# Kernel optimization log

Measured on AMD Instinct MI355X. Metric: run time of the kernel, lower is better.

## Reference

```python
import jax, jax.numpy as jnp
import numpy as np

N_NODES = 50000
N_EDGES = 800000
D_FEAT = 128      # node feature dim (== coef_dim)
COEF_DIM = 128
OUT_DIM = 128     # node_layer / neighbour_layer output dim
EPS = 1e-12       # tf.math.l2_normalize epsilon


def setup_inputs() -> dict:
    key = jax.random.key(0)
    ks = jax.random.split(key, 8)
    s = 1.0 / np.sqrt(D_FEAT)
    h = jax.random.normal(ks[0], (N_NODES, D_FEAT), dtype=jnp.float32)
    src = jax.random.randint(ks[1], (N_EDGES,), 0, N_NODES, dtype=jnp.int32)
    dst = jax.random.randint(ks[2], (N_EDGES,), 0, N_NODES, dtype=jnp.int32)
    W_coef = jax.random.normal(ks[3], (D_FEAT, COEF_DIM), dtype=jnp.float32) * s
    b_coef = jnp.zeros((COEF_DIM,), dtype=jnp.float32)
    W_red = jax.random.normal(ks[4], (2 * COEF_DIM, 1), dtype=jnp.float32) * (1.0 / np.sqrt(2 * COEF_DIM))
    b_red = jnp.zeros((1,), dtype=jnp.float32)
    W_node = jax.random.normal(ks[5], (D_FEAT, OUT_DIM), dtype=jnp.float32) * s
    b_node = jnp.zeros((OUT_DIM,), dtype=jnp.float32)
    W_neigh = jax.random.normal(ks[6], (D_FEAT, OUT_DIM), dtype=jnp.float32) * s
    b_neigh = jnp.zeros((OUT_DIM,), dtype=jnp.float32)
    return {"h": h, "src": src, "dst": dst,
            "W_coef": W_coef, "b_coef": b_coef,
            "W_red": W_red, "b_red": b_red,
            "W_node": W_node, "b_node": b_node,
            "W_neigh": W_neigh, "b_neigh": b_neigh}


def reference(h, src, dst, W_coef, b_coef, W_red, b_red, W_node, b_node, W_neigh, b_neigh):
    n = h.shape[0]
    # message func: per-edge coef transform of source features (activation=None)
    q = h @ W_coef + b_coef                      # [N, C] dst-side coef features
    m = q[src]                                   # [E, C] (coef_layer(h[src]))
    # reduce func: attention score per edge from concat(dst coef, message)
    e = jnp.concatenate([q[dst], m], axis=-1) @ W_red + b_red   # [E, 1]
    e = e[:, 0]
    # softmax over incoming edges of each destination node (stable)
    emax = jax.ops.segment_max(e, dst, num_segments=n)          # [N]
    ex = jnp.exp(e - emax[dst])                                 # [E]
    denom = jax.ops.segment_sum(ex, dst, num_segments=n)        # [N]
    alpha = ex / (denom[dst] + EPS)                             # [E]
    # weighted neighbour aggregation of raw source features ('neigh' mailbox)
    agg = jax.ops.segment_sum(alpha[:, None] * h[src], dst, num_segments=n)  # [N, D]
    # new_h = concat(node_layer(h), neighbour_layer(agg))
    new_h = jnp.concatenate([h @ W_node + b_node, agg @ W_neigh + b_neigh], axis=-1)  # [N, 2*OUT]
    # tf.math.l2_normalize along last axis
    sq = jnp.sum(new_h * new_h, axis=-1, keepdims=True)
    return new_h * jax.lax.rsqrt(jnp.maximum(sq, EPS))
```

## Files before the change

kernel.cpp:

```cpp
#include <hip/hip_runtime.h>
#include <hip/hip_bf16.h>
#include <math.h>

#define N_NODES 50000
#define N_EDGES 800000
#define D_FEAT  128
#define EPSF    1e-12f

#define OFF_U2      0
#define OFF_PARTIAL 1024
#define OFF_S       4096
#define OFF_ROWPTR  204800
#define OFF_WTN     405504
#define OFF_WTG     438272
#define OFF_SSRC    471040
#define OFF_HB      3671040
#define OFF_AGGB    16471040

typedef __attribute__((ext_vector_type(8))) short bf8;
typedef __attribute__((ext_vector_type(4))) float f4;

__global__ void make_u2_kernel(const float* __restrict__ W_coef,
                               const float* __restrict__ W_red,
                               float* __restrict__ u2) {
    __shared__ float wr[128];
    int k = threadIdx.x;
    wr[k] = W_red[128 + k];
    __syncthreads();
    const float4* row = (const float4*)(W_coef + k * 128);
    float acc = 0.f;
    #pragma unroll
    for (int j = 0; j < 32; ++j) {
        float4 v = row[j];
        acc += v.x * wr[4*j] + v.y * wr[4*j+1] + v.z * wr[4*j+2] + v.w * wr[4*j+3];
    }
    u2[k] = acc;
}

__global__ __launch_bounds__(256) void prep_kernel(
        const float* __restrict__ h, const float* __restrict__ u2,
        const float* __restrict__ Wn, const float* __restrict__ Wg,
        const int* __restrict__ dst,
        float* __restrict__ s, unsigned short* __restrict__ hb,
        unsigned short* __restrict__ WtN, unsigned short* __restrict__ WtG,
        int* __restrict__ row_ptr, int* __restrict__ rank) {
    int b = blockIdx.x;
    if (b < 12500) {
        int node = b * 4 + (threadIdx.x >> 6);
        int lane = threadIdx.x & 63;
        float2 hv = ((const float2*)(h + (size_t)node * 128))[lane];
        float2 uv = ((const float2*)u2)[lane];
        float v = hv.x * uv.x + hv.y * uv.y;
        #pragma unroll
        for (int off = 32; off; off >>= 1) v += __shfl_xor(v, off);
        if (lane == 0) s[node] = v;
        __hip_bfloat162 p = __float22bfloat162_rn(hv);
        ((unsigned int*)(hb + (size_t)node * 128))[lane] = *(unsigned int*)&p;
    } else if (b < 12564) {
        int idx = (b - 12500) * 256 + threadIdx.x;
        int n = idx >> 7, k = idx & 127;
        __hip_bfloat16 a = __float2bfloat16(Wn[k * 128 + n]);
        __hip_bfloat16 g = __float2bfloat16(Wg[k * 128 + n]);
        WtN[n * 128 + k] = *(unsigned short*)&a;
        WtG[n * 128 + k] = *(unsigned short*)&g;
    } else {
        int e = (b - 12564) * 256 + threadIdx.x;
        if (e < N_EDGES) rank[e] = atomicAdd(&row_ptr[dst[e]], 1);
    }
}

__global__ __launch_bounds__(256) void reduce_kernel(const int* __restrict__ hist,
                                                     int* __restrict__ partial) {
    int gid = blockIdx.x * 256 + threadIdx.x;
    int v = (gid < N_NODES) ? hist[gid] : 0;
    #pragma unroll
    for (int off = 32; off; off >>= 1) v += __shfl_down(v, off);
    __shared__ int ws[4];
    int lane = threadIdx.x & 63, wid = threadIdx.x >> 6;
    if (lane == 0) ws[wid] = v;
    __syncthreads();
    if (threadIdx.x == 0) partial[blockIdx.x] = ws[0] + ws[1] + ws[2] + ws[3];
}

__global__ __launch_bounds__(256) void scan_partials_kernel(int* __restrict__ partial,
                                                            int nb) {
    int tid = threadIdx.x;
    int lane = tid & 63, wid = tid >> 6;
    int v = (tid < nb) ? partial[tid] : 0;
    int incl = v;
    #pragma unroll
    for (int off = 1; off < 64; off <<= 1) {
        int t = __shfl_up(incl, off);
        if (lane >= off) incl += t;
    }
    __shared__ int ws[4];
    if (lane == 63) ws[wid] = incl;
    __syncthreads();
    __shared__ int wbase[4];
    if (tid < 4) {
        int b = 0;
        for (int i = 0; i < tid; ++i) b += ws[i];
        wbase[tid] = b;
    }
    __syncthreads();
    partial[tid] = wbase[wid] + incl - v;
}

__global__ __launch_bounds__(256) void scan_apply_kernel(
        const int* __restrict__ partial,
        int* __restrict__ row_ptr) {
    int gid = blockIdx.x * 256 + threadIdx.x;
    int tid = threadIdx.x;
    int lane = tid & 63, wid = tid >> 6;
    int v = (gid < N_NODES) ? row_ptr[gid] : 0;
    int incl = v;
    #pragma unroll
    for (int off = 1; off < 64; off <<= 1) {
        int t = __shfl_up(incl, off);
        if (lane >= off) incl += t;
    }
    __shared__ int ws[4];
    if (lane == 63) ws[wid] = incl;
    __syncthreads();
    __shared__ int wbase[4];
    if (tid < 4) {
        int b = 0;
        for (int i = 0; i < tid; ++i) b += ws[i];
        wbase[tid] = b;
    }
    __syncthreads();
    int excl = partial[blockIdx.x] + wbase[wid] + incl - v;
    if (gid < N_NODES) row_ptr[gid] = excl;
    if (gid == 0) row_ptr[N_NODES] = N_EDGES;
}

__global__ __launch_bounds__(256) void scatter_kernel(
        const int* __restrict__ src, const int* __restrict__ dst,
        const int* __restrict__ rank, const int* __restrict__ row_ptr,
        int* __restrict__ ssrc) {
    int i = blockIdx.x * 256 + threadIdx.x;
    if (i < N_EDGES / 4) {
        int4 d = ((const int4*)dst)[i];
        int4 r = ((const int4*)rank)[i];
        int4 sv = ((const int4*)src)[i];
        ssrc[row_ptr[d.x] + r.x] = sv.x;
        ssrc[row_ptr[d.y] + r.y] = sv.y;
        ssrc[row_ptr[d.z] + r.z] = sv.z;
        ssrc[row_ptr[d.w] + r.w] = sv.w;
    }
}

__global__ __launch_bounds__(256) void aggregate_kernel(
        const int* __restrict__ row_ptr, const int* __restrict__ ssrc,
        const float* __restrict__ s,
        const unsigned short* __restrict__ hb,
        unsigned short* __restrict__ aggb) {
    int node = blockIdx.x * 4 + (threadIdx.x >> 6);
    int lane = threadIdx.x & 63;
    if (node >= N_NODES) return;
    int beg = row_ptr[node];
    int deg = row_ptr[node + 1] - beg;
    int q = lane >> 4, l16 = lane & 15;

    float acc[8] = {0.f, 0.f, 0.f, 0.f, 0.f, 0.f, 0.f, 0.f};
    float denom = 0.f;
    for (int base = 0; base < deg; base += 64) {
        int cnt = min(64, deg - base);
        int esrc = 0;
        float w_l = 0.f;
        if (lane < cnt) {
            esrc = ssrc[beg + base + lane];
            w_l = __expf(s[esrc]);
        }
        denom += w_l;
        int groups = (cnt + 3) >> 2;
        for (int j = 0; j < groups; ++j) {
            int e = 4 * j + q;
            int ec = min(e, cnt - 1);
            int bsrc = __shfl(esrc, ec);
            float w = __shfl(w_l, ec);
            if (e >= cnt) w = 0.f;
            uint4 hv = *(const uint4*)(hb + (size_t)bsrc * 128 + l16 * 8);
            acc[0] = fmaf(w, __uint_as_float(hv.x << 16),        acc[0]);
            acc[1] = fmaf(w, __uint_as_float(hv.x & 0xFFFF0000u), acc[1]);
            acc[2] = fmaf(w, __uint_as_float(hv.y << 16),        acc[2]);
            acc[3] = fmaf(w, __uint_as_float(hv.y & 0xFFFF0000u), acc[3]);
            acc[4] = fmaf(w, __uint_as_float(hv.z << 16),        acc[4]);
            acc[5] = fmaf(w, __uint_as_float(hv.z & 0xFFFF0000u), acc[5]);
            acc[6] = fmaf(w, __uint_as_float(hv.w << 16),        acc[6]);
            acc[7] = fmaf(w, __uint_as_float(hv.w & 0xFFFF0000u), acc[7]);
        }
    }
    #pragma unroll
    for (int i = 0; i < 8; ++i) {
        acc[i] += __shfl_xor(acc[i], 16);
        acc[i] += __shfl_xor(acc[i], 32);
    }
    #pragma unroll
    for (int off = 32; off; off >>= 1) denom += __shfl_xor(denom, off);
    float inv = 1.f / (denom + EPSF);
    if (q == 0) {
        unsigned o[4];
        #pragma unroll
        for (int i = 0; i < 4; ++i) {
            __hip_bfloat162 p = __float22bfloat162_rn(
                make_float2(acc[2*i] * inv, acc[2*i+1] * inv));
            o[i] = *(unsigned*)&p;
        }
        *(uint4*)(aggb + (size_t)node * 128 + l16 * 8) = make_uint4(o[0], o[1], o[2], o[3]);
    }
}

__global__ __launch_bounds__(256) void gemm_norm_mfma(
        const unsigned short* __restrict__ hb, const unsigned short* __restrict__ aggb,
        const unsigned short* __restrict__ WtN, const unsigned short* __restrict__ WtG,
        const float* __restrict__ b_node, const float* __restrict__ b_neigh,
        float* __restrict__ out) {
    int wave = threadIdx.x >> 6;
    int lane = threadIdx.x & 63;
    int node0 = blockIdx.x * 64 + wave * 16;
    if (node0 >= N_NODES) return;
    int quad = lane >> 4, l16 = lane & 15;
    int arow = node0 + l16;

    f4 accN[8], accG[8];
    #pragma unroll
    for (int t = 0; t < 8; ++t) {
        accN[t] = (f4){0.f, 0.f, 0.f, 0.f};
        accG[t] = (f4){0.f, 0.f, 0.f, 0.f};
    }

    #pragma unroll
    for (int kc = 0; kc < 4; ++kc) {
        int kbase = kc * 32 + quad * 8;
        bf8 aH = *(const bf8*)(hb   + (size_t)arow * 128 + kbase);
        bf8 aG = *(const bf8*)(aggb + (size_t)arow * 128 + kbase);
        #pragma unroll
        for (int t = 0; t < 8; ++t) {
            bf8 bN = *(const bf8*)(WtN + (size_t)(t * 16 + l16) * 128 + kbase);
            bf8 bG = *(const bf8*)(WtG + (size_t)(t * 16 + l16) * 128 + kbase);
            accN[t] = __builtin_amdgcn_mfma_f32_16x16x32_bf16(aH, bN, accN[t], 0, 0, 0);
            accG[t] = __builtin_amdgcn_mfma_f32_16x16x32_bf16(aG, bG, accG[t], 0, 0, 0);
        }
    }

    float ssr[4] = {0.f, 0.f, 0.f, 0.f};
    #pragma unroll
    for (int t = 0; t < 8; ++t) {
        float bn = b_node[t * 16 + l16];
        float bg = b_neigh[t * 16 + l16];
        #pragma unroll
        for (int r = 0; r < 4; ++r) {
            accN[t][r] += bn;
            accG[t][r] += bg;
            ssr[r] = fmaf(accN[t][r], accN[t][r], ssr[r]);
            ssr[r] = fmaf(accG[t][r], accG[t][r], ssr[r]);
        }
    }
    #pragma unroll
    for (int r = 0; r < 4; ++r) {
        ssr[r] += __shfl_xor(ssr[r], 1);
        ssr[r] += __shfl_xor(ssr[r], 2);
        ssr[r] += __shfl_xor(ssr[r], 4);
        ssr[r] += __shfl_xor(ssr[r], 8);
    }
    #pragma unroll
    for (int r = 0; r < 4; ++r) {
        float sc = rsqrtf(fmaxf(ssr[r], EPSF));
        size_t node = node0 + quad * 4 + r;
        float* o = out + node * 256;
        #pragma unroll
        for (int t = 0; t < 8; ++t) {
            o[t * 16 + l16]       = accN[t][r] * sc;
            o[128 + t * 16 + l16] = accG[t][r] * sc;
        }
    }
}

extern "C" void kernel_launch(void* const* d_in, const int* in_sizes, int n_in,
                              void* d_out, int out_size, void* d_ws, size_t ws_size,
                              hipStream_t stream) {
    const float* h       = (const float*)d_in[0];
    const int*   src     = (const int*)d_in[1];
    const int*   dst     = (const int*)d_in[2];
    const float* W_coef  = (const float*)d_in[3];
    const float* W_red   = (const float*)d_in[5];
    const float* W_node  = (const float*)d_in[7];
    const float* b_node  = (const float*)d_in[8];
    const float* W_neigh = (const float*)d_in[9];
    const float* b_neigh = (const float*)d_in[10];
    float* out = (float*)d_out;

    char* w = (char*)d_ws;
    float*          u2      = (float*)(w + OFF_U2);
    int*            partial = (int*)(w + OFF_PARTIAL);
    float*          s       = (float*)(w + OFF_S);
    int*            row_ptr = (int*)(w + OFF_ROWPTR);
    unsigned short* WtN     = (unsigned short*)(w + OFF_WTN);
    unsigned short* WtG     = (unsigned short*)(w + OFF_WTG);
    int*            ssrc    = (int*)(w + OFF_SSRC);
    unsigned short* hb      = (unsigned short*)(w + OFF_HB);
    unsigned short* aggb    = (unsigned short*)(w + OFF_AGGB);
    int*            rank    = (int*)(w + OFF_AGGB);

    const int NB = (N_NODES + 255) / 256;

    hipMemsetAsync(w + OFF_ROWPTR, 0, (N_NODES + 1) * sizeof(int), stream);
    make_u2_kernel<<<1, 128, 0, stream>>>(W_coef, W_red, u2);
    prep_kernel<<<15689, 256, 0, stream>>>(h, u2, W_node, W_neigh, dst,
                                           s, hb, WtN, WtG, row_ptr, rank);
    reduce_kernel<<<NB, 256, 0, stream>>>(row_ptr, partial);
    scan_partials_kernel<<<1, 256, 0, stream>>>(partial, NB);
    scan_apply_kernel<<<NB, 256, 0, stream>>>(partial, row_ptr);
    scatter_kernel<<<(N_EDGES / 4 + 255) / 256, 256, 0, stream>>>(src, dst, rank, row_ptr, ssrc);
    aggregate_kernel<<<N_NODES / 4, 256, 0, stream>>>(row_ptr, ssrc, s, hb, aggb);
    gemm_norm_mfma<<<(N_NODES + 63) / 64, 256, 0, stream>>>(
        hb, aggb, WtN, WtG, b_node, b_neigh, out);
}
```

Measured before the change: 236.4 us.

## Replace global-atomic CSR build with two-level bucketed counting sort

Builds the destination-sorted CSR with a two-pass radix-style sort instead of one global atomic per edge into row_ptr. Edges are first binned into groups of 120 destination nodes using per-chunk LDS histograms, a column scan and a coarse scatter. Each group is then sorted locally in LDS to produce row_ptr and ssrc. This removes heavily contended global atomics and the memset, at the cost of an extra bucket pass and a serial column-scan kernel. It also packs src into 16 bits, which relies on node ids staying below 65536.

```diff
diff --git a/kernel.cpp b/kernel.cpp
--- a/kernel.cpp
+++ b/kernel.cpp
@@ -7,15 +7,23 @@
 #define D_FEAT  128
 #define EPSF    1e-12f
 
+#define NPG     120
+#define NG      417
+#define CHUNK_E 4096
+#define NCHUNK  196
+
 #define OFF_U2      0
-#define OFF_PARTIAL 1024
-#define OFF_S       4096
-#define OFF_ROWPTR  204800
-#define OFF_WTN     405504
-#define OFF_WTG     438272
-#define OFF_SSRC    471040
-#define OFF_HB      3671040
-#define OFF_AGGB    16471040
+#define OFF_GPTR    1024
+#define OFF_TOT     4096
+#define OFF_S       8192
+#define OFF_ROWPTR  208896
+#define OFF_M       409600
+#define OFF_MX      737280
+#define OFF_WTN     1064960
+#define OFF_WTG     1097728
+#define OFF_SSRC    1130496
+#define OFF_HB      4330496
+#define OFF_AGGB    17130496
 
 typedef __attribute__((ext_vector_type(8))) short bf8;
 typedef __attribute__((ext_vector_type(4))) float f4;
@@ -43,7 +51,7 @@
         const int* __restrict__ dst,
         float* __restrict__ s, unsigned short* __restrict__ hb,
         unsigned short* __restrict__ WtN, unsigned short* __restrict__ WtG,
-        int* __restrict__ row_ptr, int* __restrict__ rank) {
+        int* __restrict__ M) {
     int b = blockIdx.x;
     if (b < 12500) {
         int node = b * 4 + (threadIdx.x >> 6);
@@ -64,89 +72,124 @@
         WtN[n * 128 + k] = *(unsigned short*)&a;
         WtG[n * 128 + k] = *(unsigned short*)&g;
     } else {
-        int e = (b - 12564) * 256 + threadIdx.x;
-        if (e < N_EDGES) rank[e] = atomicAdd(&row_ptr[dst[e]], 1);
-    }
-}
-
-__global__ __launch_bounds__(256) void reduce_kernel(const int* __restrict__ hist,
-                                                     int* __restrict__ partial) {
-    int gid = blockIdx.x * 256 + threadIdx.x;
-    int v = (gid < N_NODES) ? hist[gid] : 0;
-    #pragma unroll
-    for (int off = 32; off; off >>= 1) v += __shfl_down(v, off);
-    __shared__ int ws[4];
-    int lane = threadIdx.x & 63, wid = threadIdx.x >> 6;
-    if (lane == 0) ws[wid] = v;
-    __syncthreads();
-    if (threadIdx.x == 0) partial[blockIdx.x] = ws[0] + ws[1] + ws[2] + ws[3];
-}
-
-__global__ __launch_bounds__(256) void scan_partials_kernel(int* __restrict__ partial,
-                                                            int nb) {
+        __shared__ int lh[NG];
+        int chunk = b - 12564;
+        int tid = threadIdx.x;
+        for (int i = tid; i < NG; i += 256) lh[i] = 0;
+        __syncthreads();
+        int base_e = chunk * CHUNK_E;
+        #pragma unroll
+        for (int it = 0; it < CHUNK_E / 256; ++it) {
+            int e = base_e + it * 256 + tid;
+            if (e < N_EDGES) atomicAdd(&lh[(unsigned)dst[e] / NPG], 1);
+        }
+        __syncthreads();
+        for (int i = tid; i < NG; i += 256) M[chunk * NG + i] = lh[i];
+    }
+}
+
+__global__ __launch_bounds__(256) void mcol_kernel(
+        const int* __restrict__ M, int* __restrict__ Mx,
+        int* __restrict__ totals) {
+    int g = blockIdx.x * 256 + threadIdx.x;
+    if (g >= NG) return;
+    int running = 0;
+    for (int b = 0; b < NCHUNK; ++b) {
+        int v = M[b * NG + g];
+        Mx[b * NG + g] = running;
+        running += v;
+    }
+    totals[g] = running;
+}
+
+__global__ __launch_bounds__(512) void scan_gptr_kernel(
+        const int* __restrict__ totals, int* __restrict__ gptr) {
     int tid = threadIdx.x;
     int lane = tid & 63, wid = tid >> 6;
-    int v = (tid < nb) ? partial[tid] : 0;
+    int v = (tid < NG) ? totals[tid] : 0;
     int incl = v;
     #pragma unroll
     for (int off = 1; off < 64; off <<= 1) {
         int t = __shfl_up(incl, off);
         if (lane >= off) incl += t;
     }
-    __shared__ int ws[4];
+    __shared__ int ws[8];
     if (lane == 63) ws[wid] = incl;
     __syncthreads();
-    __shared__ int wbase[4];
-    if (tid < 4) {
+    __shared__ int wbase[8];
+    if (tid < 8) {
         int b = 0;
         for (int i = 0; i < tid; ++i) b += ws[i];
         wbase[tid] = b;
     }
     __syncthreads();
-    partial[tid] = wbase[wid] + incl - v;
-}
-
-__global__ __launch_bounds__(256) void scan_apply_kernel(
-        const int* __restrict__ partial,
-        int* __restrict__ row_ptr) {
-    int gid = blockIdx.x * 256 + threadIdx.x;
-    int tid = threadIdx.x;
+    if (tid <= NG) {
+        if (tid < NG) gptr[tid] = wbase[wid] + incl - v;
+    }
+    if (tid == 0) gptr[NG] = N_EDGES;
+}
+
+__global__ __launch_bounds__(256) void coarse_scatter_kernel(
+        const int* __restrict__ src, const int* __restrict__ dst,
+        const int* __restrict__ Mx, const int* __restrict__ gptr,
+        int* __restrict__ bucket) {
+    __shared__ int base[NG];
+    __shared__ int cnt[NG];
+    int b = blockIdx.x, tid = threadIdx.x;
+    for (int i = tid; i < NG; i += 256) {
+        base[i] = Mx[b * NG + i] + gptr[i];
+        cnt[i] = 0;
+    }
+    __syncthreads();
+    int base_e = b * CHUNK_E;
+    #pragma unroll
+    for (int it = 0; it < CHUNK_E / 256; ++it) {
+        int e = base_e + it * 256 + tid;
+        if (e < N_EDGES) {
+            int d = dst[e];
+            int g = (unsigned)d / NPG;
+            int r = atomicAdd(&cnt[g], 1);
+            bucket[base[g] + r] = src[e] | ((d - g * NPG) << 16);
+        }
+    }
+}
+
+__global__ __launch_bounds__(128) void fine_kernel(
+        const int* __restrict__ gptr, const int* __restrict__ bucket,
+        int* __restrict__ row_ptr, int* __restrict__ ssrc) {
+    __shared__ int cnt[NPG];
+    __shared__ int cnt2[NPG];
+    __shared__ int sexcl[NPG];
+    __shared__ int ws[2];
+    int g = blockIdx.x, tid = threadIdx.x;
+    if (tid < NPG) { cnt[tid] = 0; cnt2[tid] = 0; }
+    __syncthreads();
+    int beg = gptr[g], end = gptr[g + 1];
+    for (int i = beg + tid; i < end; i += 128)
+        atomicAdd(&cnt[bucket[i] >> 16], 1);
+    __syncthreads();
     int lane = tid & 63, wid = tid >> 6;
-    int v = (gid < N_NODES) ? row_ptr[gid] : 0;
+    int v = (tid < NPG) ? cnt[tid] : 0;
     int incl = v;
     #pragma unroll
     for (int off = 1; off < 64; off <<= 1) {
         int t = __shfl_up(incl, off);
         if (lane >= off) incl += t;
     }
-    __shared__ int ws[4];
     if (lane == 63) ws[wid] = incl;
     __syncthreads();
-    __shared__ int wbase[4];
-    if (tid < 4) {
-        int b = 0;
-        for (int i = 0; i < tid; ++i) b += ws[i];
-        wbase[tid] = b;
-    }
-    __syncthreads();
-    int excl = partial[blockIdx.x] + wbase[wid] + incl - v;
-    if (gid < N_NODES) row_ptr[gid] = excl;
-    if (gid == 0) row_ptr[N_NODES] = N_EDGES;
-}
-
-__global__ __launch_bounds__(256) void scatter_kernel(
-        const int* __restrict__ src, const int* __restrict__ dst,
-        const int* __restrict__ rank, const int* __restrict__ row_ptr,
-        int* __restrict__ ssrc) {
-    int i = blockIdx.x * 256 + threadIdx.x;
-    if (i < N_EDGES / 4) {
-        int4 d = ((const int4*)dst)[i];
-        int4 r = ((const int4*)rank)[i];
-        int4 sv = ((const int4*)src)[i];
-        ssrc[row_ptr[d.x] + r.x] = sv.x;
-        ssrc[row_ptr[d.y] + r.y] = sv.y;
-        ssrc[row_ptr[d.z] + r.z] = sv.z;
-        ssrc[row_ptr[d.w] + r.w] = sv.w;
+    if (wid == 1) incl += ws[0];
+    int excl = incl - v;
+    if (tid < NPG) sexcl[tid] = excl;
+    int node = g * NPG + tid;
+    if (tid < NPG && node < N_NODES) row_ptr[node] = beg + excl;
+    if (g == NG - 1 && tid == 0) row_ptr[N_NODES] = N_EDGES;
+    __syncthreads();
+    for (int i = beg + tid; i < end; i += 128) {
+        int p = bucket[i];
+        int loc = p >> 16;
+        int r = atomicAdd(&cnt2[loc], 1);
+        ssrc[beg + sexcl[loc] + r] = p & 0xFFFF;
     }
 }
 
@@ -293,26 +336,26 @@
 
     char* w = (char*)d_ws;
     float*          u2      = (float*)(w + OFF_U2);
-    int*            partial = (int*)(w + OFF_PARTIAL);
+    int*            gptr    = (int*)(w + OFF_GPTR);
+    int*            totals  = (int*)(w + OFF_TOT);
     float*          s       = (float*)(w + OFF_S);
     int*            row_ptr = (int*)(w + OFF_ROWPTR);
+    int*            M       = (int*)(w + OFF_M);
+    int*            Mx      = (int*)(w + OFF_MX);
     unsigned short* WtN     = (unsigned short*)(w + OFF_WTN);
     unsigned short* WtG     = (unsigned short*)(w + OFF_WTG);
     int*            ssrc    = (int*)(w + OFF_SSRC);
     unsigned short* hb      = (unsigned short*)(w + OFF_HB);
     unsigned short* aggb    = (unsigned short*)(w + OFF_AGGB);
-    int*            rank    = (int*)(w + OFF_AGGB);
-
-    const int NB = (N_NODES + 255) / 256;
-
-    hipMemsetAsync(w + OFF_ROWPTR, 0, (N_NODES + 1) * sizeof(int), stream);
+    int*            bucket  = (int*)(w + OFF_AGGB);
+
     make_u2_kernel<<<1, 128, 0, stream>>>(W_coef, W_red, u2);
-    prep_kernel<<<15689, 256, 0, stream>>>(h, u2, W_node, W_neigh, dst,
-                                           s, hb, WtN, WtG, row_ptr, rank);
-    reduce_kernel<<<NB, 256, 0, stream>>>(row_ptr, partial);
-    scan_partials_kernel<<<1, 256, 0, stream>>>(partial, NB);
-    scan_apply_kernel<<<NB, 256, 0, stream>>>(partial, row_ptr);
-    scatter_kernel<<<(N_EDGES / 4 + 255) / 256, 256, 0, stream>>>(src, dst, rank, row_ptr, ssrc);
+    prep_kernel<<<12500 + 64 + NCHUNK, 256, 0, stream>>>(
+        h, u2, W_node, W_neigh, dst, s, hb, WtN, WtG, M);
+    mcol_kernel<<<(NG + 255) / 256, 256, 0, stream>>>(M, Mx, totals);
+    scan_gptr_kernel<<<1, 512, 0, stream>>>(totals, gptr);
+    coarse_scatter_kernel<<<NCHUNK, 256, 0, stream>>>(src, dst, Mx, gptr, bucket);
+    fine_kernel<<<NG, 128, 0, stream>>>(gptr, bucket, row_ptr, ssrc);
     aggregate_kernel<<<N_NODES / 4, 256, 0, stream>>>(row_ptr, ssrc, s, hb, aggb);
     gemm_norm_mfma<<<(N_NODES + 63) / 64, 256, 0, stream>>>(
         hb, aggb, WtN, WtG, b_node, b_neigh, out);
```

Result: faster. 220.1 us (-6.9%).
